# Performance work log

Hardware: AMD Instinct MI355X
Metric: run time of the kernel (lower is better)

The kernel has to match this reference:

```python
import jax, jax.numpy as jnp
import numpy as np

DIL = 1  # dilation


def setup_inputs() -> dict:
    key = jax.random.key(0)
    k0, k1, k2, k3 = jax.random.split(key, 4)
    B, Cin, Cout, K, L, NR = 16, 256, 256, 3, 4096, 5
    x = jax.random.normal(k0, (B, Cin, L), jnp.float32)
    # kaiming-uniform-ish scale for conv kernels
    base_kernels = jax.random.normal(k1, (NR, Cout, Cin, K), jnp.float32) * (1.0 / np.sqrt(Cin * K))
    base_biases = jax.random.normal(k2, (NR, Cout), jnp.float32) * (1.0 / np.sqrt(Cin * K))
    # controller: Linear(Cin*K -> NR) followed by softmax over rules
    ctrl_w = jax.random.normal(k3, (Cin * K, NR), jnp.float32) * (1.0 / np.sqrt(Cin * K))
    ctrl_b = jnp.zeros((NR,), jnp.float32)
    return {"x": x, "base_kernels": base_kernels, "base_biases": base_biases,
            "ctrl_w": ctrl_w, "ctrl_b": ctrl_b}


def reference(x, base_kernels, base_biases, ctrl_w, ctrl_b):
    NR, Cout, Cin, K = base_kernels.shape
    B, _, L = x.shape
    pad = (K - 1) * DIL
    px = jnp.pad(x, ((0, 0), (0, 0), (pad, 0)))  # causal left pad -> (B, Cin, L+pad)

    # patches: padded_x.unfold(dim=2, size=K, step=1)[:, :, :L] -> (B, Cin, L, K)
    patches = jnp.stack([px[:, :, k:k + L] for k in range(K)], axis=-1)
    patches = patches.transpose(0, 2, 1, 3).reshape(B, L, Cin * K)  # (B, L, Cin*K)

    # controller -> normalized firing strengths (B, L, NR)
    fr = jax.nn.softmax(patches @ ctrl_w + ctrl_b, axis=-1)

    # all n_rules causal convs in one grouped-as-batched-output conv
    rhs = base_kernels.reshape(NR * Cout, Cin, K)
    conv = jax.lax.conv_general_dilated(
        px, rhs, window_strides=(1,), padding=[(0, 0)],
        rhs_dilation=(DIL,), dimension_numbers=("NCH", "OIH", "NCH"))  # (B, NR*Cout, L)
    conv = conv.reshape(B, NR, Cout, L) + base_biases[None, :, :, None]

    # weighted sum over experts: sum_n fr[b,l,n] * conv[b,n,o,l]
    return jnp.einsum("bnol,bln->bol", conv, fr)
```

## Files before the change

kernel.cpp:

```cpp
#include <hip/hip_runtime.h>
#include <hip/hip_bf16.h>

typedef __attribute__((ext_vector_type(4))) float floatx4;
typedef __attribute__((ext_vector_type(8))) short shortx8;

#define NB   16
#define CIN  256
#define COUT 256
#define KW   3
#define LL   4096
#define NR   5
#define QK   768
#define NP   65536

static __device__ __forceinline__ unsigned short bf16bits(float f) {
    __hip_bfloat16 h = __float2bfloat16(f);
    return __builtin_bit_cast(unsigned short, h);
}

static __device__ __forceinline__ void gload16(const void* g, void* l) {
    __builtin_amdgcn_global_load_lds(
        (const __attribute__((address_space(1))) void*)g,
        (__attribute__((address_space(3))) void*)l, 16, 0, 0);
}

__global__ void k_transpose(const float* __restrict__ x, __hip_bfloat16* __restrict__ xt) {
    __shared__ float t[64][65];
    int l0 = blockIdx.x * 64, c0 = blockIdx.y * 64, b = blockIdx.z;
    int tid = threadIdx.x;
    int r16 = tid >> 4, q16 = tid & 15;
    #pragma unroll
    for (int pass = 0; pass < 4; ++pass) {
        int cin = pass * 16 + r16;
        float4 v = *(const float4*)&x[((size_t)(b * CIN + c0 + cin)) * LL + l0 + q16 * 4];
        t[q16 * 4 + 0][cin] = v.x;
        t[q16 * 4 + 1][cin] = v.y;
        t[q16 * 4 + 2][cin] = v.z;
        t[q16 * 4 + 3][cin] = v.w;
    }
    __syncthreads();
    #pragma unroll
    for (int pass = 0; pass < 4; ++pass) {
        int lr = pass * 16 + r16;
        int c4 = q16 * 4;
        ushort4 u;
        u.x = bf16bits(t[lr][c4 + 0]);
        u.y = bf16bits(t[lr][c4 + 1]);
        u.z = bf16bits(t[lr][c4 + 2]);
        u.w = bf16bits(t[lr][c4 + 3]);
        *(ushort4*)&xt[((size_t)(b * LL + l0 + lr)) * CIN + c0 + c4] = u;
    }
}

__global__ void k_wprep(const float* __restrict__ bk, __hip_bfloat16* __restrict__ wb) {
    int i = blockIdx.x * 256 + threadIdx.x;
    if (i >= NR * COUT * QK) return;
    int m = i / QK, q = i % QK;
    int o = (m / 80) * 16 + (m & 15);
    int r = (m % 80) / 16;
    int k = q >> 8, cin = q & 255;
    wb[i] = __float2bfloat16(bk[((r * COUT + o) * CIN + cin) * KW + k]);
}

__global__ void k_fr(const float* __restrict__ x, const float* __restrict__ cw,
                     const float* __restrict__ cb, float* __restrict__ fr) {
    __shared__ float xsh[128][68];
    __shared__ float cws[QK * NR];
    __shared__ float part[4][64][NR];
    int p0 = blockIdx.x * 64;
    int b = p0 >> 12, l0 = p0 & (LL - 1);
    int tid = threadIdx.x, lane = tid & 63, wid = tid >> 6;
    for (int i = tid; i < QK * NR; i += 256) cws[i] = cw[i];
    float lg[NR] = {0.f, 0.f, 0.f, 0.f, 0.f};
    for (int ch = 0; ch < 2; ++ch) {
        __syncthreads();
        for (int i = tid; i < 128 * 17; i += 256) {
            int cl = i / 17, c4 = (i % 17) * 4;
            int gl = l0 - 4 + c4;
            float4 v = make_float4(0.f, 0.f, 0.f, 0.f);
            if (gl >= 0) v = *(const float4*)&x[((size_t)(b * CIN + ch * 128 + cl)) * LL + gl];
            *(float4*)&xsh[cl][c4] = v;
        }
        __syncthreads();
        #pragma unroll 8
        for (int r = 0; r < 32; ++r) {
            int cl = wid * 32 + r;
            int cg = ch * 128 + cl;
            float x0 = xsh[cl][lane + 2], x1 = xsh[cl][lane + 3], x2 = xsh[cl][lane + 4];
            const float* w = &cws[cg * 3 * NR];
            #pragma unroll
            for (int n = 0; n < NR; ++n)
                lg[n] += x0 * w[n] + x1 * w[NR + n] + x2 * w[2 * NR + n];
        }
    }
    #pragma unroll
    for (int n = 0; n < NR; ++n) part[wid][lane][n] = lg[n];
    __syncthreads();
    if (tid < 64) {
        float l2[NR];
        #pragma unroll
        for (int n = 0; n < NR; ++n)
            l2[n] = cb[n] + part[0][tid][n] + part[1][tid][n] + part[2][tid][n] + part[3][tid][n];
        float m = l2[0];
        #pragma unroll
        for (int n = 1; n < NR; ++n) m = fmaxf(m, l2[n]);
        float e[NR], s = 0.f;
        #pragma unroll
        for (int n = 0; n < NR; ++n) { e[n] = __expf(l2[n] - m); s += e[n]; }
        float inv = 1.f / s;
        #pragma unroll
        for (int n = 0; n < NR; ++n) fr[(size_t)(p0 + tid) * NR + n] = e[n] * inv;
    }
}

#define BUFSH 15936
#define WOFFS 8256
__global__ __launch_bounds__(256, 2)
void k_conv(const __hip_bfloat16* __restrict__ xt, const __hip_bfloat16* __restrict__ wb,
            const float* __restrict__ fr, const float* __restrict__ bias,
            float* __restrict__ out) {
    __shared__ __align__(16) short lds[2 * BUFSH];
    __shared__ float bs[80];

    int g = blockIdx.x;
    int pt = ((g >> 7) << 3) | (g & 7);
    int y  = (g >> 3) & 15;
    int p0 = pt * 256;
    int m0 = y * 80, o0 = y * 16;
    int b = p0 >> 12, l0 = p0 & (LL - 1);
    int tid = threadIdx.x;
    int lane = tid & 63, wn = tid >> 6;
    int quad = lane >> 4, l16 = lane & 15;

    const __hip_bfloat16* xb = xt + (size_t)b * (LL * CIN);

    if (tid < 80) bs[tid] = bias[(tid >> 4) * COUT + o0 + (tid & 15)];

    int xsrc[4];
    #pragma unroll
    for (int j = 0; j < 4; ++j) {
        int i = tid + j * 256;
        int rowp = i >> 2, cslot = i & 3;
        int cg = cslot ^ ((rowp + 2) & 3);
        xsrc[j] = (l0 + rowp) * CIN + cg * 8;
    }
    int wsrc[4];
    #pragma unroll
    for (int j = 0; j < 4; ++j) {
        int i = tid + j * 256;
        int s = i >> 2, cslot = i & 3;
        int cg = cslot ^ (s & 3);
        int kh = s / 80, m = s - kh * 80;
        wsrc[j] = (i < 960) ? ((m0 + m) * QK + kh * 256 + cg * 8) : 0;
    }
    int hR = tid >> 2, hslot = tid & 3;
    int hcg = hslot ^ (hR & 3);
    int hsrc = (l0 - 2 + hR) * CIN + hcg * 8;

    int boff[3][4], aoff[3][5];
    #pragma unroll
    for (int kh = 0; kh < 3; ++kh) {
        #pragma unroll
        for (int nf = 0; nf < 4; ++nf) {
            int row = wn * 64 + nf * 16 + l16 + kh;
            int phys = quad ^ (row & 3);
            boff[kh][nf] = row * 32 + phys * 8;
        }
        #pragma unroll
        for (int mf = 0; mf < NR; ++mf) {
            int s = kh * 80 + mf * 16 + l16;
            int phys = quad ^ (s & 3);
            aoff[kh][mf] = WOFFS + s * 32 + phys * 8;
        }
    }

    floatx4 acc[NR][4];
    #pragma unroll
    for (int mf = 0; mf < NR; ++mf)
        #pragma unroll
        for (int nf = 0; nf < 4; ++nf)
            acc[mf][nf] = (floatx4){0.f, 0.f, 0.f, 0.f};

    auto stage = [&](short* B, int ph) {
        const __hip_bfloat16* xp = xb + ph * 32;
        const __hip_bfloat16* wp = wb + ph * 32;
        uint4 hv = make_uint4(0u, 0u, 0u, 0u);
        if (l0 > 0 && tid < 8) hv = *(const uint4*)(xp + hsrc);
        #pragma unroll
        for (int j = 0; j < 4; ++j)
            gload16(xp + xsrc[j], B + 64 + (j * 256 + wn * 64) * 8);
        #pragma unroll
        for (int j = 0; j < 3; ++j)
            gload16(wp + wsrc[j], B + WOFFS + (j * 256 + wn * 64) * 8);
        if (wn < 3)
            gload16(wp + wsrc[3], B + WOFFS + (768 + wn * 64) * 8);
        if (tid < 8) *(uint4*)(B + tid * 8) = hv;
    };

    auto compute = [&](const short* B) {
        #pragma unroll
        for (int kh = 0; kh < 3; ++kh) {
            shortx8 bfrag[4], afrag[NR];
            #pragma unroll
            for (int nf = 0; nf < 4; ++nf)
                bfrag[nf] = *(const shortx8*)&B[boff[kh][nf]];
            #pragma unroll
            for (int mf = 0; mf < NR; ++mf)
                afrag[mf] = *(const shortx8*)&B[aoff[kh][mf]];
            #pragma unroll
            for (int mf = 0; mf < NR; ++mf)
                #pragma unroll
                for (int nf = 0; nf < 4; ++nf)
                    acc[mf][nf] = __builtin_amdgcn_mfma_f32_16x16x32_bf16(
                        afrag[mf], bfrag[nf], acc[mf][nf], 0, 0, 0);
        }
    };

    stage(&lds[0], 0);
    __syncthreads();
    for (int ph = 0; ph < 8; ph += 2) {
        stage(&lds[BUFSH], ph + 1);
        compute(&lds[0]);
        __syncthreads();
        if (ph < 6) stage(&lds[0], ph + 2);
        compute(&lds[BUFSH]);
        __syncthreads();
    }

    #pragma unroll
    for (int nf = 0; nf < 4; ++nf) {
        int colp = wn * 64 + nf * 16 + l16;
        const float* fp = fr + (size_t)(p0 + colp) * NR;
        float f0 = fp[0], f1 = fp[1], f2 = fp[2], f3 = fp[3], f4 = fp[4];
        #pragma unroll
        for (int j = 0; j < 4; ++j) {
            int olo = quad * 4 + j;
            float v = f0 * (acc[0][nf][j] + bs[0 * 16 + olo])
                    + f1 * (acc[1][nf][j] + bs[1 * 16 + olo])
                    + f2 * (acc[2][nf][j] + bs[2 * 16 + olo])
                    + f3 * (acc[3][nf][j] + bs[3 * 16 + olo])
                    + f4 * (acc[4][nf][j] + bs[4 * 16 + olo]);
            out[((size_t)(b * COUT + o0 + olo)) * LL + l0 + colp] = v;
        }
    }
}

extern "C" void kernel_launch(void* const* d_in, const int* in_sizes, int n_in,
                              void* d_out, int out_size, void* d_ws, size_t ws_size,
                              hipStream_t stream) {
    const float* x  = (const float*)d_in[0];
    const float* bk = (const float*)d_in[1];
    const float* bb = (const float*)d_in[2];
    const float* cw = (const float*)d_in[3];
    const float* cb = (const float*)d_in[4];
    float* out = (float*)d_out;

    char* ws = (char*)d_ws;
    __hip_bfloat16* xt = (__hip_bfloat16*)ws;
    __hip_bfloat16* wb = (__hip_bfloat16*)(ws + 33554432);
    float*          fr = (float*)(ws + 33554432 + 1966080);

    k_transpose<<<dim3(LL / 64, CIN / 64, NB), dim3(256), 0, stream>>>(x, xt);
    k_wprep<<<dim3((NR * COUT * QK + 255) / 256), dim3(256), 0, stream>>>(bk, wb);
    k_fr<<<dim3(NP / 64), dim3(256), 0, stream>>>(x, cw, cb, fr);
    k_conv<<<dim3(NP / 256 * (COUT / 16)), dim3(256), 0, stream>>>(xt, wb, fr, bb, out);
}
```

Baseline: 278.7 us.

## Fuse controller logits into transpose kernel and change LDS swizzle pattern

The controller logit computation now runs inside the transpose kernel, reusing the tile already held in shared memory, so x is read once instead of twice. Partial logits per 64-channel slice are combined with atomic adds into a buffer that the weight-prep kernel zeroes, and a separate small kernel applies the softmax. Separately, the conv kernel's LDS XOR swizzle now keys on row>>1 instead of row, to change the bank-conflict pattern of the MFMA operand reads. The cost is extra atomics and one more launch.

```diff
diff --git a/kernel.cpp b/kernel.cpp
--- a/kernel.cpp
+++ b/kernel.cpp
@@ -24,36 +24,10 @@
         (__attribute__((address_space(3))) void*)l, 16, 0, 0);
 }
 
-__global__ void k_transpose(const float* __restrict__ x, __hip_bfloat16* __restrict__ xt) {
-    __shared__ float t[64][65];
-    int l0 = blockIdx.x * 64, c0 = blockIdx.y * 64, b = blockIdx.z;
-    int tid = threadIdx.x;
-    int r16 = tid >> 4, q16 = tid & 15;
-    #pragma unroll
-    for (int pass = 0; pass < 4; ++pass) {
-        int cin = pass * 16 + r16;
-        float4 v = *(const float4*)&x[((size_t)(b * CIN + c0 + cin)) * LL + l0 + q16 * 4];
-        t[q16 * 4 + 0][cin] = v.x;
-        t[q16 * 4 + 1][cin] = v.y;
-        t[q16 * 4 + 2][cin] = v.z;
-        t[q16 * 4 + 3][cin] = v.w;
-    }
-    __syncthreads();
-    #pragma unroll
-    for (int pass = 0; pass < 4; ++pass) {
-        int lr = pass * 16 + r16;
-        int c4 = q16 * 4;
-        ushort4 u;
-        u.x = bf16bits(t[lr][c4 + 0]);
-        u.y = bf16bits(t[lr][c4 + 1]);
-        u.z = bf16bits(t[lr][c4 + 2]);
-        u.w = bf16bits(t[lr][c4 + 3]);
-        *(ushort4*)&xt[((size_t)(b * LL + l0 + lr)) * CIN + c0 + c4] = u;
-    }
-}
-
-__global__ void k_wprep(const float* __restrict__ bk, __hip_bfloat16* __restrict__ wb) {
+__global__ void k_wprep(const float* __restrict__ bk, __hip_bfloat16* __restrict__ wb,
+                        float* __restrict__ frz) {
     int i = blockIdx.x * 256 + threadIdx.x;
+    if (i < NP * NR) frz[i] = 0.f;
     if (i >= NR * COUT * QK) return;
     int m = i / QK, q = i % QK;
     int o = (m / 80) * 16 + (m & 15);
@@ -62,55 +36,83 @@
     wb[i] = __float2bfloat16(bk[((r * COUT + o) * CIN + cin) * KW + k]);
 }
 
-__global__ void k_fr(const float* __restrict__ x, const float* __restrict__ cw,
-                     const float* __restrict__ cb, float* __restrict__ fr) {
-    __shared__ float xsh[128][68];
-    __shared__ float cws[QK * NR];
-    __shared__ float part[4][64][NR];
-    int p0 = blockIdx.x * 64;
-    int b = p0 >> 12, l0 = p0 & (LL - 1);
-    int tid = threadIdx.x, lane = tid & 63, wid = tid >> 6;
-    for (int i = tid; i < QK * NR; i += 256) cws[i] = cw[i];
+__global__ void k_tfr(const float* __restrict__ x, const float* __restrict__ cw,
+                      __hip_bfloat16* __restrict__ xt, float* __restrict__ logit) {
+    __shared__ float t[66][65];
+    __shared__ float cwsh[64 * 15];
+    int l0 = blockIdx.x * 64, c0 = blockIdx.y * 64, b = blockIdx.z;
+    int tid = threadIdx.x;
+    int r16 = tid >> 4, q16 = tid & 15;
+
+    for (int i = tid; i < 64 * 15; i += 256) cwsh[i] = cw[c0 * 15 + i];
+
+    #pragma unroll
+    for (int pass = 0; pass < 4; ++pass) {
+        int cin = pass * 16 + r16;
+        float4 v = *(const float4*)&x[((size_t)(b * CIN + c0 + cin)) * LL + l0 + q16 * 4];
+        t[q16 * 4 + 2][cin] = v.x;
+        t[q16 * 4 + 3][cin] = v.y;
+        t[q16 * 4 + 4][cin] = v.z;
+        t[q16 * 4 + 5][cin] = v.w;
+    }
+    if (tid < 128) {
+        int cin = tid >> 1, j = tid & 1;
+        float v = 0.f;
+        if (l0 > 0) v = x[((size_t)(b * CIN + c0 + cin)) * LL + l0 - 2 + j];
+        t[j][cin] = v;
+    }
+    __syncthreads();
+
+    #pragma unroll
+    for (int pass = 0; pass < 4; ++pass) {
+        int lr = pass * 16 + r16;
+        int c4 = q16 * 4;
+        ushort4 u;
+        u.x = bf16bits(t[lr + 2][c4 + 0]);
+        u.y = bf16bits(t[lr + 2][c4 + 1]);
+        u.z = bf16bits(t[lr + 2][c4 + 2]);
+        u.w = bf16bits(t[lr + 2][c4 + 3]);
+        *(ushort4*)&xt[((size_t)(b * LL + l0 + lr)) * CIN + c0 + c4] = u;
+    }
+
+    int p = tid >> 2, q = tid & 3;
     float lg[NR] = {0.f, 0.f, 0.f, 0.f, 0.f};
-    for (int ch = 0; ch < 2; ++ch) {
-        __syncthreads();
-        for (int i = tid; i < 128 * 17; i += 256) {
-            int cl = i / 17, c4 = (i % 17) * 4;
-            int gl = l0 - 4 + c4;
-            float4 v = make_float4(0.f, 0.f, 0.f, 0.f);
-            if (gl >= 0) v = *(const float4*)&x[((size_t)(b * CIN + ch * 128 + cl)) * LL + gl];
-            *(float4*)&xsh[cl][c4] = v;
-        }
-        __syncthreads();
-        #pragma unroll 8
-        for (int r = 0; r < 32; ++r) {
-            int cl = wid * 32 + r;
-            int cg = ch * 128 + cl;
-            float x0 = xsh[cl][lane + 2], x1 = xsh[cl][lane + 3], x2 = xsh[cl][lane + 4];
-            const float* w = &cws[cg * 3 * NR];
-            #pragma unroll
-            for (int n = 0; n < NR; ++n)
-                lg[n] += x0 * w[n] + x1 * w[NR + n] + x2 * w[2 * NR + n];
-        }
-    }
-    #pragma unroll
-    for (int n = 0; n < NR; ++n) part[wid][lane][n] = lg[n];
-    __syncthreads();
-    if (tid < 64) {
-        float l2[NR];
+    #pragma unroll 4
+    for (int ci = 0; ci < 16; ++ci) {
+        int cin = q * 16 + ci;
+        float x0 = t[p][cin], x1 = t[p + 1][cin], x2 = t[p + 2][cin];
+        const float* w = &cwsh[cin * 15];
         #pragma unroll
         for (int n = 0; n < NR; ++n)
-            l2[n] = cb[n] + part[0][tid][n] + part[1][tid][n] + part[2][tid][n] + part[3][tid][n];
-        float m = l2[0];
-        #pragma unroll
-        for (int n = 1; n < NR; ++n) m = fmaxf(m, l2[n]);
-        float e[NR], s = 0.f;
-        #pragma unroll
-        for (int n = 0; n < NR; ++n) { e[n] = __expf(l2[n] - m); s += e[n]; }
-        float inv = 1.f / s;
-        #pragma unroll
-        for (int n = 0; n < NR; ++n) fr[(size_t)(p0 + tid) * NR + n] = e[n] * inv;
-    }
+            lg[n] += x0 * w[n] + x1 * w[5 + n] + x2 * w[10 + n];
+    }
+    #pragma unroll
+    for (int n = 0; n < NR; ++n) {
+        lg[n] += __shfl_xor(lg[n], 1);
+        lg[n] += __shfl_xor(lg[n], 2);
+    }
+    if (q == 0) {
+        float* lp = &logit[(size_t)(b * LL + l0 + p) * NR];
+        #pragma unroll
+        for (int n = 0; n < NR; ++n) atomicAdd(&lp[n], lg[n]);
+    }
+}
+
+__global__ void k_softmax(const float* __restrict__ cb, float* __restrict__ fr) {
+    int p = blockIdx.x * 256 + threadIdx.x;
+    if (p >= NP) return;
+    float l2[NR];
+    #pragma unroll
+    for (int n = 0; n < NR; ++n) l2[n] = fr[(size_t)p * NR + n] + cb[n];
+    float m = l2[0];
+    #pragma unroll
+    for (int n = 1; n < NR; ++n) m = fmaxf(m, l2[n]);
+    float e[NR], s = 0.f;
+    #pragma unroll
+    for (int n = 0; n < NR; ++n) { e[n] = __expf(l2[n] - m); s += e[n]; }
+    float inv = 1.f / s;
+    #pragma unroll
+    for (int n = 0; n < NR; ++n) fr[(size_t)p * NR + n] = e[n] * inv;
 }
 
 #define BUFSH 15936
@@ -141,7 +143,7 @@
     for (int j = 0; j < 4; ++j) {
         int i = tid + j * 256;
         int rowp = i >> 2, cslot = i & 3;
-        int cg = cslot ^ ((rowp + 2) & 3);
+        int cg = cslot ^ (((rowp + 2) >> 1) & 3);
         xsrc[j] = (l0 + rowp) * CIN + cg * 8;
     }
     int wsrc[4];
@@ -149,12 +151,12 @@
     for (int j = 0; j < 4; ++j) {
         int i = tid + j * 256;
         int s = i >> 2, cslot = i & 3;
-        int cg = cslot ^ (s & 3);
+        int cg = cslot ^ ((s >> 1) & 3);
         int kh = s / 80, m = s - kh * 80;
         wsrc[j] = (i < 960) ? ((m0 + m) * QK + kh * 256 + cg * 8) : 0;
     }
     int hR = tid >> 2, hslot = tid & 3;
-    int hcg = hslot ^ (hR & 3);
+    int hcg = hslot;
     int hsrc = (l0 - 2 + hR) * CIN + hcg * 8;
 
     int boff[3][4], aoff[3][5];
@@ -163,13 +165,13 @@
         #pragma unroll
         for (int nf = 0; nf < 4; ++nf) {
             int row = wn * 64 + nf * 16 + l16 + kh;
-            int phys = quad ^ (row & 3);
+            int phys = quad ^ ((row >> 1) & 3);
             boff[kh][nf] = row * 32 + phys * 8;
         }
         #pragma unroll
         for (int mf = 0; mf < NR; ++mf) {
             int s = kh * 80 + mf * 16 + l16;
-            int phys = quad ^ (s & 3);
+            int phys = quad ^ ((s >> 1) & 3);
             aoff[kh][mf] = WOFFS + s * 32 + phys * 8;
         }
     }
@@ -260,8 +262,8 @@
     __hip_bfloat16* wb = (__hip_bfloat16*)(ws + 33554432);
     float*          fr = (float*)(ws + 33554432 + 1966080);
 
-    k_transpose<<<dim3(LL / 64, CIN / 64, NB), dim3(256), 0, stream>>>(x, xt);
-    k_wprep<<<dim3((NR * COUT * QK + 255) / 256), dim3(256), 0, stream>>>(bk, wb);
-    k_fr<<<dim3(NP / 64), dim3(256), 0, stream>>>(x, cw, cb, fr);
+    k_wprep<<<dim3((NR * COUT * QK + 255) / 256), dim3(256), 0, stream>>>(bk, wb, fr);
+    k_tfr<<<dim3(LL / 64, CIN / 64, NB), dim3(256), 0, stream>>>(x, cw, xt, fr);
+    k_softmax<<<dim3(NP / 256), dim3(256), 0, stream>>>(cb, fr);
     k_conv<<<dim3(NP / 256 * (COUT / 16)), dim3(256), 0, stream>>>(xt, wb, fr, bb, out);
 }
```

Result: faster. 264.4 us (-5.2%).
